# Performance work log

Measured on AMD Instinct MI355X. Metric: run time of the kernel, lower is better.

Reference implementation:

```python
import jax, jax.numpy as jnp
import numpy as np

NEG = -1e9  # stands in for -inf; sparsemax thresholding makes these entries exactly 0


def sparsemax(z):
    """Sparsemax along the last axis (Martins & Astudillo 2016)."""
    K = z.shape[-1]
    z_sorted = -jnp.sort(-z, axis=-1)                      # descending
    kk = jnp.arange(1, K + 1, dtype=z.dtype)
    z_cum = jnp.cumsum(z_sorted, axis=-1)
    support = 1.0 + kk * z_sorted > z_cum                  # [..., K] bool
    k_sup = jnp.sum(support, axis=-1, keepdims=True).astype(z.dtype)
    z_sum = jnp.sum(jnp.where(support, z_sorted, 0.0), axis=-1, keepdims=True)
    tau = (z_sum - 1.0) / k_sup
    return jnp.maximum(z - tau, 0.0)


def setup_inputs() -> dict:
    key = jax.random.key(0)
    ks = jax.random.split(key, 7)
    b, t, e, h = 8, 1024, 128, 8
    x = jax.random.normal(ks[0], (b, t, e), dtype=jnp.float32)
    mask = jax.random.randint(ks[1], (b, t, t), 0, 2, dtype=jnp.int32)
    w_q = jax.random.normal(ks[2], (e, h * e), dtype=jnp.float32) * 0.05
    w_k = jax.random.normal(ks[3], (e, h * e), dtype=jnp.float32) * 0.05
    w_v = jax.random.normal(ks[4], (e, h * e), dtype=jnp.float32) * 0.05
    w_s = jax.random.normal(ks[5], (h, e), dtype=jnp.float32) * 0.05
    b_s = jnp.zeros((h,), dtype=jnp.float32)
    return {"x": x, "mask": mask, "w_q": w_q, "w_k": w_k, "w_v": w_v,
            "w_s": w_s, "b_s": b_s}


def reference(x, mask, w_q, w_k, w_v, w_s, b_s):
    b, t, e = x.shape
    h = w_s.shape[0]
    scale = 1.0 / jnp.sqrt(jnp.asarray(e, x.dtype))  # temperature = emb_dim**0.5

    # projections: each head gets FULL emb_dim width (per original module)
    q = (x @ w_q).reshape(b, t, h, e).transpose(2, 0, 1, 3)  # [h,b,t,e]
    k = (x @ w_k).reshape(b, t, h, e).transpose(2, 0, 1, 3)
    v = (x @ w_v).reshape(b, t, h, e).transpose(2, 0, 1, 3)

    attn = jnp.einsum('hbqe,hbke->hbqk', q * scale, k)       # [h,b,t,t]

    m = mask.astype(bool)[None]                              # [1,b,t,t], broadcast over heads
    inf_mask = jnp.all(m, axis=-1, keepdims=True)            # rows fully masked
    attn = jnp.where(m, NEG, attn)
    attn = jnp.where(inf_mask, 0.0, attn)
    attn = sparsemax(attn)
    attn = jnp.where(inf_mask, 0.0, attn)                    # dropout is identity (p=0)

    out = jnp.einsum('hbqk,hbke->hbqe', attn, v)             # [h,b,t,e]
    out = out.transpose(1, 2, 0, 3)                          # [b,t,h,e]

    sel = jax.nn.softmax(jnp.mean(x, axis=1) @ w_s.T + b_s, axis=-1)  # [b,h]
    return jnp.einsum('bh,bthe->bte', sel, out)              # gated head mix
```

## Files before the change

kernel.cpp:

```cpp
#include <hip/hip_runtime.h>
#include <hip/hip_bf16.h>
#include <math.h>

#define SCALE 0.08838834764831845f

using short8  = __attribute__((ext_vector_type(8))) short;
using short4v = __attribute__((ext_vector_type(4))) short;
using us4     = __attribute__((ext_vector_type(4))) unsigned short;
using f32x4   = __attribute__((ext_vector_type(4))) float;
typedef unsigned long long u64;
typedef unsigned short ushort_t;

static __device__ __forceinline__ ushort_t bf16_of(float f) {
    __hip_bfloat16 h = __float2bfloat16(f);
    return *reinterpret_cast<ushort_t*>(&h);
}
static __device__ __forceinline__ float f_of_bf16(unsigned int u) {
    union { unsigned int i; float f; } v; v.i = u << 16; return v.f;
}

__global__ __launch_bounds__(256)
void prep_all(const float* __restrict__ x, ushort_t* __restrict__ xb,
              const float* __restrict__ wq, const float* __restrict__ wk,
              const float* __restrict__ wv, ushort_t* __restrict__ Wt,
              const int* __restrict__ mask, u64* __restrict__ mp) {
    __shared__ float tile[64][129];
    const int bx = blockIdx.x;
    const int tid = threadIdx.x;
    if (bx < 1024) {
        const int i = bx * 256 + tid;
        float4 v = reinterpret_cast<const float4*>(x)[i];
        short4v o;
        o.x = (short)bf16_of(v.x); o.y = (short)bf16_of(v.y);
        o.z = (short)bf16_of(v.z); o.w = (short)bf16_of(v.w);
        reinterpret_cast<short4v*>(xb)[i] = o;
    } else if (bx < 1072) {
        const int wb = bx - 1024;
        const int mat = wb >> 4;
        const int n0 = (wb & 15) * 64;
        const float* W = (mat == 0) ? wq : (mat == 1) ? wk : wv;
        for (int idx = tid; idx < 8192; idx += 256) {
            const int k = idx >> 6, c = idx & 63;
            tile[c][k] = W[(size_t)k * 1024 + n0 + c];
        }
        __syncthreads();
        for (int idx = tid; idx < 8192; idx += 256) {
            const int c = idx >> 7, k = idx & 127;
            Wt[(size_t)(mat * 1024 + n0 + c) * 128 + k] = bf16_of(tile[c][k]);
        }
    } else {
        const int mb = bx - 1072;
        const int row = mb * 4 + (tid >> 6);
        const int l = tid & 63;
        const int* m = mask + (size_t)row * 1024;
        #pragma unroll
        for (int c = 0; c < 16; ++c) {
            u64 bm = __ballot(m[c * 64 + l] != 0);
            if (l == 0) mp[(size_t)row * 16 + c] = bm;
        }
    }
}

__global__ __launch_bounds__(256)
void proj_gemm(const ushort_t* __restrict__ xb, const ushort_t* __restrict__ Wt,
               ushort_t* __restrict__ Q, ushort_t* __restrict__ K,
               ushort_t* __restrict__ V) {
    const int tid = threadIdx.x;
    const int w = tid >> 6, l = tid & 63;
    const int l15 = l & 15, lq = l >> 4;
    const int m0 = blockIdx.x * 64;
    const int nb = blockIdx.y;
    const int mat = nb >> 4;
    const int n0 = (nb & 15) * 64;
    const int b = m0 >> 10;

    short8 af[4][4];
    #pragma unroll
    for (int at = 0; at < 4; ++at) {
        const ushort_t* ar = xb + (size_t)(m0 + at * 16 + l15) * 128 + lq * 8;
        #pragma unroll
        for (int f = 0; f < 4; ++f)
            af[at][f] = *reinterpret_cast<const short8*>(ar + f * 32);
    }
    const int ng = n0 + w * 16 + l15;
    const ushort_t* br = Wt + (size_t)(mat * 1024 + ng) * 128 + lq * 8;
    short8 bf[4];
    #pragma unroll
    for (int f = 0; f < 4; ++f)
        bf[f] = *reinterpret_cast<const short8*>(br + f * 32);
    f32x4 acc[4];
    #pragma unroll
    for (int at = 0; at < 4; ++at) acc[at] = (f32x4){0.f, 0.f, 0.f, 0.f};
    #pragma unroll
    for (int at = 0; at < 4; ++at)
        #pragma unroll
        for (int f = 0; f < 4; ++f)
            acc[at] = __builtin_amdgcn_mfma_f32_16x16x32_bf16(af[at][f], bf[f], acc[at], 0, 0, 0);

    const int h = ng >> 7, e = ng & 127;
    ushort_t* O = (mat == 0) ? Q : (mat == 1) ? K : V;
    const float scl = (mat == 0) ? SCALE : 1.0f;
    const size_t obase = (size_t)(h * 8 + b) * 131072 + e;
    #pragma unroll
    for (int at = 0; at < 4; ++at)
        #pragma unroll
        for (int r = 0; r < 4; ++r) {
            const int t = (m0 & 1023) + at * 16 + lq * 4 + r;
            O[obase + (size_t)t * 128] = bf16_of(acc[at][r] * scl);
        }
}

__global__ __launch_bounds__(1024)
void sel_kernel(const float* __restrict__ x, const float* __restrict__ wsl,
                const float* __restrict__ bsl, float* __restrict__ sel) {
    __shared__ float part[8][128];
    __shared__ float xm[128];
    __shared__ float lg[8];
    const int b = blockIdx.x;
    const int tid = threadIdx.x;
    const int e = tid & 127, tc = tid >> 7;
    float s = 0.f;
    for (int t = 0; t < 128; ++t)
        s += x[((size_t)b * 1024 + tc * 128 + t) * 128 + e];
    part[tc][e] = s;
    __syncthreads();
    if (tid < 128) {
        float tot = 0.f;
        #pragma unroll
        for (int i = 0; i < 8; ++i) tot += part[i][tid];
        xm[tid] = tot * (1.0f / 1024.0f);
    }
    __syncthreads();
    if (tid < 8) {
        float d = 0.f;
        for (int e2 = 0; e2 < 128; ++e2) d += xm[e2] * wsl[tid * 128 + e2];
        lg[tid] = d + bsl[tid];
    }
    __syncthreads();
    if (tid == 0) {
        float mx = lg[0];
        for (int hh = 1; hh < 8; ++hh) mx = fmaxf(mx, lg[hh]);
        float se = 0.f; float ex[8];
        for (int hh = 0; hh < 8; ++hh) { ex[hh] = expf(lg[hh] - mx); se += ex[hh]; }
        for (int hh = 0; hh < 8; ++hh) sel[b * 8 + hh] = ex[hh] / se;
    }
}

__global__ __launch_bounds__(512, 4)
void attn_kernel(const ushort_t* __restrict__ Qb, const ushort_t* __restrict__ Kb,
                 const ushort_t* __restrict__ Vb, const u64* __restrict__ mp,
                 const float* __restrict__ sel, float* __restrict__ out) {
    __shared__ float S[16 * 1024];
    __shared__ int cnt[16];
    unsigned int* list = reinterpret_cast<unsigned int*>(S);

    const int tid = threadIdx.x;
    const int w = tid >> 6, l = tid & 63;
    const int l15 = l & 15, lq = l >> 4;
    const int orig = (int)blockIdx.x;
    const int swz = (orig & 7) * 64 + (orig >> 3);
    const int b = swz >> 6;
    const int qt = swz & 63;
    const int t0 = qt * 16;
    const int rowbase = b * 1024 + t0;

    const int qrow = 2 * w + (l & 1);
    const int lh = l >> 1;
    const int prow = tid >> 5;
    const int eq = tid & 31;

    if (tid < 16) cnt[tid] = 0;

    u64 mw0[4], mw1[4];
    #pragma unroll
    for (int r = 0; r < 4; ++r) {
        const u64* mrow = mp + (size_t)(rowbase + lq * 4 + r) * 16 + w * 2;
        mw0[r] = mrow[0];
        mw1[r] = mrow[1];
    }

    f32x4 oac = {0.f, 0.f, 0.f, 0.f};

    for (int h = 0; h < 8; ++h) {
        const size_t base = (size_t)(h * 8 + b) * 131072;
        __syncthreads();

        short8 qa[4];
        {
            const ushort_t* qrp = Qb + base + (size_t)(t0 + l15) * 128 + lq * 8;
            #pragma unroll
            for (int f = 0; f < 4; ++f)
                qa[f] = *reinterpret_cast<const short8*>(qrp + f * 32);
        }

        f32x4 sc[8];
        #pragma unroll
        for (int i = 0; i < 8; ++i) {
            const int kt = w * 8 + i;
            const ushort_t* krow = Kb + base + (size_t)(kt * 16 + l15) * 128 + lq * 8;
            f32x4 acc = {0.f, 0.f, 0.f, 0.f};
            #pragma unroll
            for (int f = 0; f < 4; ++f) {
                short8 kb = *reinterpret_cast<const short8*>(krow + f * 32);
                acc = __builtin_amdgcn_mfma_f32_16x16x32_bf16(qa[f], kb, acc, 0, 0, 0);
            }
            sc[i] = acc;
        }

        #pragma unroll
        for (int r = 0; r < 4; ++r) {
            #pragma unroll
            for (int i = 0; i < 8; ++i) {
                const u64 mword = (i < 4) ? mw0[r] : mw1[r];
                const int bit = (i & 3) * 16 + l15;
                if ((mword >> bit) & 1ULL) sc[i][r] = -1e30f;
            }
        }

        #pragma unroll
        for (int r = 0; r < 4; ++r) {
            const int q = lq * 4 + r;
            #pragma unroll
            for (int i = 0; i < 8; ++i) {
                const int c = (w * 8 + i) * 4 + (l15 >> 2);
                const int cp = c ^ ((c >> 3) & 7) ^ (q & 7);
                S[q * 1024 + cp * 4 + (l15 & 3)] = sc[i][r];
            }
        }
        __syncthreads();

        float z[32];
        #pragma unroll
        for (int j = 0; j < 8; ++j) {
            const int c = lh + 32 * j;
            const int cp = c ^ ((c >> 3) & 7) ^ (qrow & 7);
            float4 v = *reinterpret_cast<const float4*>(&S[qrow * 1024 + cp * 4]);
            z[4 * j + 0] = v.x; z[4 * j + 1] = v.y;
            z[4 * j + 2] = v.z; z[4 * j + 3] = v.w;
        }

        float m16[16];
        #pragma unroll
        for (int j = 0; j < 16; ++j) m16[j] = fmaxf(z[j], z[j + 16]);
        #pragma unroll
        for (int j = 0; j < 8; ++j) m16[j] = fmaxf(m16[j], m16[j + 8]);
        #pragma unroll
        for (int j = 0; j < 4; ++j) m16[j] = fmaxf(m16[j], m16[j + 4]);
        float mx = fmaxf(fmaxf(m16[0], m16[1]), fmaxf(m16[2], m16[3]));
        #pragma unroll
        for (int mm = 2; mm < 64; mm <<= 1) mx = fmaxf(mx, __shfl_xor(mx, mm));

        float tau;
        if (mx < -1e29f) {
            tau = 3e38f;
        } else {
            tau = mx - 1.0f;
            unsigned prev = 0xFFFFFFFFu;
            for (int it = 0; it < 64; ++it) {
                float s2 = 0.f; unsigned c2 = 0u;
                #pragma unroll
                for (int k = 0; k < 32; ++k) {
                    const float zz = z[k];
                    s2 += (zz > tau) ? zz : 0.f;
                    c2 += (zz > tau) ? 1u : 0u;
                }
                #pragma unroll
                for (int mm = 2; mm < 64; mm <<= 1) {
                    s2 += __shfl_xor(s2, mm);
                    c2 += __shfl_xor(c2, mm);
                }
                if (c2 == prev) break;
                tau = (s2 - 1.f) / (float)c2;
                prev = c2;
            }
        }

        #pragma unroll
        for (int jj = 0; jj < 32; ++jj) {
            const float p = z[jj] - tau;
            if (p > 0.f) {
                const int k = 4 * lh + 128 * (jj >> 2) + (jj & 3);
                const int pos = atomicAdd(&cnt[qrow], 1);
                list[qrow * 1024 + pos] = (unsigned int)k | ((unsigned int)bf16_of(p) << 16);
            }
        }

        const float gsel = sel[b * 8 + h];
        const int n = cnt[prow];
        const ushort_t* Vrow = Vb + base;
        const unsigned int* lrow = list + prow * 1024;
        for (int j = 0; j < n; ++j) {
            const unsigned int ent = lrow[j];
            const int k = (int)(ent & 0xFFFFu);
            const float gp = gsel * f_of_bf16(ent >> 16);
            us4 vv = *reinterpret_cast<const us4*>(Vrow + (size_t)k * 128 + eq * 4);
            oac[0] += gp * f_of_bf16(vv.x);
            oac[1] += gp * f_of_bf16(vv.y);
            oac[2] += gp * f_of_bf16(vv.z);
            oac[3] += gp * f_of_bf16(vv.w);
        }
        if (eq == 0) cnt[prow] = 0;
    }

    float* orow = out + ((size_t)(b * 1024 + t0 + prow)) * 128 + eq * 4;
    *reinterpret_cast<float4*>(orow) = (float4){oac[0], oac[1], oac[2], oac[3]};
}

extern "C" void kernel_launch(void* const* d_in, const int* in_sizes, int n_in,
                              void* d_out, int out_size, void* d_ws, size_t ws_size,
                              hipStream_t stream) {
    (void)in_sizes; (void)n_in; (void)ws_size; (void)out_size;
    const float* x   = (const float*)d_in[0];
    const int* mask  = (const int*)d_in[1];
    const float* wq  = (const float*)d_in[2];
    const float* wk  = (const float*)d_in[3];
    const float* wv  = (const float*)d_in[4];
    const float* wsl = (const float*)d_in[5];
    const float* bsl = (const float*)d_in[6];
    float* out = (float*)d_out;

    char* wsc = (char*)d_ws;
    float*    sel = (float*)wsc;
    u64*      mp  = (u64*)(wsc + 4096);
    ushort_t* xb  = (ushort_t*)(wsc + 4096 + 1048576);
    ushort_t* Wt  = (ushort_t*)(wsc + 4096 + 1048576 + 2097152);
    ushort_t* Qb  = (ushort_t*)(wsc + 4096 + 1048576 + 2097152 + 786432);
    ushort_t* Kb  = Qb + (size_t)8388608;
    ushort_t* Vb  = Kb + (size_t)8388608;

    prep_all<<<3120, 256, 0, stream>>>(x, xb, wq, wk, wv, Wt, mask, mp);
    sel_kernel<<<8, 1024, 0, stream>>>(x, wsl, bsl, sel);
    proj_gemm<<<dim3(128, 48), 256, 0, stream>>>(xb, Wt, Qb, Kb, Vb);
    attn_kernel<<<512, 512, 0, stream>>>(Qb, Kb, Vb, mp, sel, out);
}
```

Before: 268.1 us.

## Double attention block threads to 1024 with one wave per query row

The attention kernel now launches 1024 threads per block (16 waves). Each wave computes 4 key tiles of scores instead of 8, and owns exactly one query row for the sparsemax threshold search and the sparse V accumulation, so each lane handles 16 scores and 2 output columns. The block-index swizzle is dropped, so consecutive blocks now map to different batches. The change adds thread-level parallelism and shortens each thread's serial work. In exchange it costs more full-wave shuffle reductions and higher register pressure under the tighter launch bounds.

Measured after the change: 328.3 us. +22.4%, slower.

```diff
diff --git a/kernel.cpp b/kernel.cpp
--- a/kernel.cpp
+++ b/kernel.cpp
@@ -6,7 +6,7 @@
 
 using short8  = __attribute__((ext_vector_type(8))) short;
 using short4v = __attribute__((ext_vector_type(4))) short;
-using us4     = __attribute__((ext_vector_type(4))) unsigned short;
+using us2     = __attribute__((ext_vector_type(2))) unsigned short;
 using f32x4   = __attribute__((ext_vector_type(4))) float;
 typedef unsigned long long u64;
 typedef unsigned short ushort_t;
@@ -146,7 +146,7 @@
     }
 }
 
-__global__ __launch_bounds__(512, 4)
+__global__ __launch_bounds__(1024, 8)
 void attn_kernel(const ushort_t* __restrict__ Qb, const ushort_t* __restrict__ Kb,
                  const ushort_t* __restrict__ Vb, const u64* __restrict__ mp,
                  const float* __restrict__ sel, float* __restrict__ out) {
@@ -155,31 +155,23 @@
     unsigned int* list = reinterpret_cast<unsigned int*>(S);
 
     const int tid = threadIdx.x;
-    const int w = tid >> 6, l = tid & 63;
-    const int l15 = l & 15, lq = l >> 4;
+    const int w = tid >> 6;
+    const int l = tid & 63;
+    const int l15 = l & 15, lq = (l >> 4) & 3;
     const int orig = (int)blockIdx.x;
-    const int swz = (orig & 7) * 64 + (orig >> 3);
-    const int b = swz >> 6;
-    const int qt = swz & 63;
+    const int b = orig & 7;
+    const int qt = orig >> 3;
     const int t0 = qt * 16;
     const int rowbase = b * 1024 + t0;
 
-    const int qrow = 2 * w + (l & 1);
-    const int lh = l >> 1;
-    const int prow = tid >> 5;
-    const int eq = tid & 31;
-
     if (tid < 16) cnt[tid] = 0;
 
-    u64 mw0[4], mw1[4];
-    #pragma unroll
-    for (int r = 0; r < 4; ++r) {
-        const u64* mrow = mp + (size_t)(rowbase + lq * 4 + r) * 16 + w * 2;
-        mw0[r] = mrow[0];
-        mw1[r] = mrow[1];
-    }
-
-    f32x4 oac = {0.f, 0.f, 0.f, 0.f};
+    u64 mw[4];
+    #pragma unroll
+    for (int r = 0; r < 4; ++r)
+        mw[r] = mp[(size_t)(rowbase + lq * 4 + r) * 16 + w];
+
+    float o0 = 0.f, o1 = 0.f;
 
     for (int h = 0; h < 8; ++h) {
         const size_t base = (size_t)(h * 8 + b) * 131072;
@@ -193,10 +185,10 @@
                 qa[f] = *reinterpret_cast<const short8*>(qrp + f * 32);
         }
 
-        f32x4 sc[8];
-        #pragma unroll
-        for (int i = 0; i < 8; ++i) {
-            const int kt = w * 8 + i;
+        f32x4 sc[4];
+        #pragma unroll
+        for (int i = 0; i < 4; ++i) {
+            const int kt = 4 * w + i;
             const ushort_t* krow = Kb + base + (size_t)(kt * 16 + l15) * 128 + lq * 8;
             f32x4 acc = {0.f, 0.f, 0.f, 0.f};
             #pragma unroll
@@ -210,10 +202,9 @@
         #pragma unroll
         for (int r = 0; r < 4; ++r) {
             #pragma unroll
-            for (int i = 0; i < 8; ++i) {
-                const u64 mword = (i < 4) ? mw0[r] : mw1[r];
-                const int bit = (i & 3) * 16 + l15;
-                if ((mword >> bit) & 1ULL) sc[i][r] = -1e30f;
+            for (int i = 0; i < 4; ++i) {
+                const int bit = i * 16 + l15;
+                if ((mw[r] >> bit) & 1ULL) sc[i][r] = -1e30f;
             }
         }
 
@@ -221,34 +212,32 @@
         for (int r = 0; r < 4; ++r) {
             const int q = lq * 4 + r;
             #pragma unroll
-            for (int i = 0; i < 8; ++i) {
-                const int c = (w * 8 + i) * 4 + (l15 >> 2);
+            for (int i = 0; i < 4; ++i) {
+                const int c = 16 * w + 4 * i + (l15 >> 2);
                 const int cp = c ^ ((c >> 3) & 7) ^ (q & 7);
                 S[q * 1024 + cp * 4 + (l15 & 3)] = sc[i][r];
             }
         }
         __syncthreads();
 
-        float z[32];
-        #pragma unroll
-        for (int j = 0; j < 8; ++j) {
-            const int c = lh + 32 * j;
-            const int cp = c ^ ((c >> 3) & 7) ^ (qrow & 7);
-            float4 v = *reinterpret_cast<const float4*>(&S[qrow * 1024 + cp * 4]);
+        float z[16];
+        #pragma unroll
+        for (int j = 0; j < 4; ++j) {
+            const int c = l + 64 * j;
+            const int cp = c ^ ((c >> 3) & 7) ^ (w & 7);
+            float4 v = *reinterpret_cast<const float4*>(&S[w * 1024 + cp * 4]);
             z[4 * j + 0] = v.x; z[4 * j + 1] = v.y;
             z[4 * j + 2] = v.z; z[4 * j + 3] = v.w;
         }
 
-        float m16[16];
-        #pragma unroll
-        for (int j = 0; j < 16; ++j) m16[j] = fmaxf(z[j], z[j + 16]);
-        #pragma unroll
-        for (int j = 0; j < 8; ++j) m16[j] = fmaxf(m16[j], m16[j + 8]);
-        #pragma unroll
-        for (int j = 0; j < 4; ++j) m16[j] = fmaxf(m16[j], m16[j + 4]);
-        float mx = fmaxf(fmaxf(m16[0], m16[1]), fmaxf(m16[2], m16[3]));
-        #pragma unroll
-        for (int mm = 2; mm < 64; mm <<= 1) mx = fmaxf(mx, __shfl_xor(mx, mm));
+        float m8[8];
+        #pragma unroll
+        for (int j = 0; j < 8; ++j) m8[j] = fmaxf(z[j], z[j + 8]);
+        #pragma unroll
+        for (int j = 0; j < 4; ++j) m8[j] = fmaxf(m8[j], m8[j + 4]);
+        float mx = fmaxf(fmaxf(m8[0], m8[1]), fmaxf(m8[2], m8[3]));
+        #pragma unroll
+        for (int mm = 1; mm < 64; mm <<= 1) mx = fmaxf(mx, __shfl_xor(mx, mm));
 
         float tau;
         if (mx < -1e29f) {
@@ -259,13 +248,13 @@
             for (int it = 0; it < 64; ++it) {
                 float s2 = 0.f; unsigned c2 = 0u;
                 #pragma unroll
-                for (int k = 0; k < 32; ++k) {
+                for (int k = 0; k < 16; ++k) {
                     const float zz = z[k];
                     s2 += (zz > tau) ? zz : 0.f;
                     c2 += (zz > tau) ? 1u : 0u;
                 }
                 #pragma unroll
-                for (int mm = 2; mm < 64; mm <<= 1) {
+                for (int mm = 1; mm < 64; mm <<= 1) {
                     s2 += __shfl_xor(s2, mm);
                     c2 += __shfl_xor(c2, mm);
                 }
@@ -276,34 +265,32 @@
         }
 
         #pragma unroll
-        for (int jj = 0; jj < 32; ++jj) {
+        for (int jj = 0; jj < 16; ++jj) {
             const float p = z[jj] - tau;
             if (p > 0.f) {
-                const int k = 4 * lh + 128 * (jj >> 2) + (jj & 3);
-                const int pos = atomicAdd(&cnt[qrow], 1);
-                list[qrow * 1024 + pos] = (unsigned int)k | ((unsigned int)bf16_of(p) << 16);
+                const int k = 4 * l + 256 * (jj >> 2) + (jj & 3);
+                const int pos = atomicAdd(&cnt[w], 1);
+                list[w * 1024 + pos] = (unsigned int)k | ((unsigned int)bf16_of(p) << 16);
             }
         }
 
         const float gsel = sel[b * 8 + h];
-        const int n = cnt[prow];
+        const int n = cnt[w];
         const ushort_t* Vrow = Vb + base;
-        const unsigned int* lrow = list + prow * 1024;
+        const unsigned int* lrow = list + w * 1024;
         for (int j = 0; j < n; ++j) {
             const unsigned int ent = lrow[j];
             const int k = (int)(ent & 0xFFFFu);
             const float gp = gsel * f_of_bf16(ent >> 16);
-            us4 vv = *reinterpret_cast<const us4*>(Vrow + (size_t)k * 128 + eq * 4);
-            oac[0] += gp * f_of_bf16(vv.x);
-            oac[1] += gp * f_of_bf16(vv.y);
-            oac[2] += gp * f_of_bf16(vv.z);
-            oac[3] += gp * f_of_bf16(vv.w);
-        }
-        if (eq == 0) cnt[prow] = 0;
-    }
-
-    float* orow = out + ((size_t)(b * 1024 + t0 + prow)) * 128 + eq * 4;
-    *reinterpret_cast<float4*>(orow) = (float4){oac[0], oac[1], oac[2], oac[3]};
+            us2 vv = *reinterpret_cast<const us2*>(Vrow + (size_t)k * 128 + 2 * l);
+            o0 += gp * f_of_bf16(vv.x);
+            o1 += gp * f_of_bf16(vv.y);
+        }
+        if (l == 0) cnt[w] = 0;
+    }
+
+    float* orow = out + ((size_t)(b * 1024 + t0 + w)) * 128 + 2 * l;
+    *reinterpret_cast<float2*>(orow) = (float2){o0, o1};
 }
 
 extern "C" void kernel_launch(void* const* d_in, const int* in_sizes, int n_in,
@@ -331,5 +318,5 @@
     prep_all<<<3120, 256, 0, stream>>>(x, xb, wq, wk, wv, Wt, mask, mp);
     sel_kernel<<<8, 1024, 0, stream>>>(x, wsl, bsl, sel);
     proj_gemm<<<dim3(128, 48), 256, 0, stream>>>(xb, Wt, Qb, Kb, Vb);
-    attn_kernel<<<512, 512, 0, stream>>>(Qb, Kb, Vb, mp, sel, out);
-}
+    attn_kernel<<<512, 1024, 0, stream>>>(Qb, Kb, Vb, mp, sel, out);
+}
```

## Prefetch next head's QK scores, fuse x-mean into prep, unroll PV gather

Applied to the files above, without the earlier changes.

The attention kernel now computes the QK^T MFMA scores for the next head while the current head's sparsemax and PV gather run, giving the two phases a chance to overlap. The x column-mean reduction for the head selector is moved into the prep kernel via shared and global atomics, replacing the standalone strided sel_kernel with a small finalize kernel plus a memset. The sparse PV gather loop is unrolled by two with separate accumulators to raise memory-level parallelism. In exchange, register pressure rises from the extra scn buffer, which may hurt occupancy, and the float atomic summation order becomes nondeterministic.

New measurement: 373.2 us. +39.2%, slower.

```diff
diff --git a/kernel.cpp b/kernel.cpp
--- a/kernel.cpp
+++ b/kernel.cpp
@@ -23,8 +23,10 @@
 void prep_all(const float* __restrict__ x, ushort_t* __restrict__ xb,
               const float* __restrict__ wq, const float* __restrict__ wk,
               const float* __restrict__ wv, ushort_t* __restrict__ Wt,
-              const int* __restrict__ mask, u64* __restrict__ mp) {
+              const int* __restrict__ mask, u64* __restrict__ mp,
+              float* __restrict__ xsum) {
     __shared__ float tile[64][129];
+    __shared__ float csum[128];
     const int bx = blockIdx.x;
     const int tid = threadIdx.x;
     if (bx < 1024) {
@@ -34,6 +36,15 @@
         o.x = (short)bf16_of(v.x); o.y = (short)bf16_of(v.y);
         o.z = (short)bf16_of(v.z); o.w = (short)bf16_of(v.w);
         reinterpret_cast<short4v*>(xb)[i] = o;
+        if (tid < 128) csum[tid] = 0.f;
+        __syncthreads();
+        const int e0 = (tid & 31) * 4;
+        atomicAdd(&csum[e0 + 0], v.x);
+        atomicAdd(&csum[e0 + 1], v.y);
+        atomicAdd(&csum[e0 + 2], v.z);
+        atomicAdd(&csum[e0 + 3], v.w);
+        __syncthreads();
+        if (tid < 128) atomicAdd(&xsum[(bx >> 7) * 128 + tid], csum[tid]);
     } else if (bx < 1072) {
         const int wb = bx - 1024;
         const int mat = wb >> 4;
@@ -110,30 +121,18 @@
         }
 }
 
-__global__ __launch_bounds__(1024)
-void sel_kernel(const float* __restrict__ x, const float* __restrict__ wsl,
-                const float* __restrict__ bsl, float* __restrict__ sel) {
-    __shared__ float part[8][128];
+__global__ __launch_bounds__(128)
+void sel_final(const float* __restrict__ xsum, const float* __restrict__ wsl,
+               const float* __restrict__ bsl, float* __restrict__ sel) {
     __shared__ float xm[128];
     __shared__ float lg[8];
     const int b = blockIdx.x;
     const int tid = threadIdx.x;
-    const int e = tid & 127, tc = tid >> 7;
-    float s = 0.f;
-    for (int t = 0; t < 128; ++t)
-        s += x[((size_t)b * 1024 + tc * 128 + t) * 128 + e];
-    part[tc][e] = s;
-    __syncthreads();
-    if (tid < 128) {
-        float tot = 0.f;
-        #pragma unroll
-        for (int i = 0; i < 8; ++i) tot += part[i][tid];
-        xm[tid] = tot * (1.0f / 1024.0f);
-    }
+    xm[tid] = xsum[b * 128 + tid] * (1.0f / 1024.0f);
     __syncthreads();
     if (tid < 8) {
         float d = 0.f;
-        for (int e2 = 0; e2 < 128; ++e2) d += xm[e2] * wsl[tid * 128 + e2];
+        for (int e = 0; e < 128; ++e) d += xm[e] * wsl[tid * 128 + e];
         lg[tid] = d + bsl[tid];
     }
     __syncthreads();
@@ -179,25 +178,18 @@
         mw1[r] = mrow[1];
     }
 
-    f32x4 oac = {0.f, 0.f, 0.f, 0.f};
-
-    for (int h = 0; h < 8; ++h) {
-        const size_t base = (size_t)(h * 8 + b) * 131072;
-        __syncthreads();
-
+    f32x4 sc[8];
+    {
+        const size_t base0 = (size_t)b * 131072;
         short8 qa[4];
-        {
-            const ushort_t* qrp = Qb + base + (size_t)(t0 + l15) * 128 + lq * 8;
-            #pragma unroll
-            for (int f = 0; f < 4; ++f)
-                qa[f] = *reinterpret_cast<const short8*>(qrp + f * 32);
-        }
-
-        f32x4 sc[8];
+        const ushort_t* qrp = Qb + base0 + (size_t)(t0 + l15) * 128 + lq * 8;
+        #pragma unroll
+        for (int f = 0; f < 4; ++f)
+            qa[f] = *reinterpret_cast<const short8*>(qrp + f * 32);
         #pragma unroll
         for (int i = 0; i < 8; ++i) {
             const int kt = w * 8 + i;
-            const ushort_t* krow = Kb + base + (size_t)(kt * 16 + l15) * 128 + lq * 8;
+            const ushort_t* krow = Kb + base0 + (size_t)(kt * 16 + l15) * 128 + lq * 8;
             f32x4 acc = {0.f, 0.f, 0.f, 0.f};
             #pragma unroll
             for (int f = 0; f < 4; ++f) {
@@ -206,6 +198,13 @@
             }
             sc[i] = acc;
         }
+    }
+
+    f32x4 oac = {0.f, 0.f, 0.f, 0.f};
+
+    #pragma unroll
+    for (int h = 0; h < 8; ++h) {
+        const size_t base = (size_t)(h * 8 + b) * 131072;
 
         #pragma unroll
         for (int r = 0; r < 4; ++r) {
@@ -216,6 +215,8 @@
                 if ((mword >> bit) & 1ULL) sc[i][r] = -1e30f;
             }
         }
+
+        __syncthreads();
 
         #pragma unroll
         for (int r = 0; r < 4; ++r) {
@@ -237,6 +238,28 @@
             float4 v = *reinterpret_cast<const float4*>(&S[qrow * 1024 + cp * 4]);
             z[4 * j + 0] = v.x; z[4 * j + 1] = v.y;
             z[4 * j + 2] = v.z; z[4 * j + 3] = v.w;
+        }
+
+        f32x4 scn[8];
+        if (h < 7) {
+            const size_t nbase = (size_t)((h + 1) * 8 + b) * 131072;
+            short8 qn[4];
+            const ushort_t* qrp = Qb + nbase + (size_t)(t0 + l15) * 128 + lq * 8;
+            #pragma unroll
+            for (int f = 0; f < 4; ++f)
+                qn[f] = *reinterpret_cast<const short8*>(qrp + f * 32);
+            #pragma unroll
+            for (int i = 0; i < 8; ++i) {
+                const int kt = w * 8 + i;
+                const ushort_t* krow = Kb + nbase + (size_t)(kt * 16 + l15) * 128 + lq * 8;
+                f32x4 acc = {0.f, 0.f, 0.f, 0.f};
+                #pragma unroll
+                for (int f = 0; f < 4; ++f) {
+                    short8 kb = *reinterpret_cast<const short8*>(krow + f * 32);
+                    acc = __builtin_amdgcn_mfma_f32_16x16x32_bf16(qn[f], kb, acc, 0, 0, 0);
+                }
+                scn[i] = acc;
+            }
         }
 
         float m16[16];
@@ -289,17 +312,40 @@
         const int n = cnt[prow];
         const ushort_t* Vrow = Vb + base;
         const unsigned int* lrow = list + prow * 1024;
-        for (int j = 0; j < n; ++j) {
-            const unsigned int ent = lrow[j];
-            const int k = (int)(ent & 0xFFFFu);
-            const float gp = gsel * f_of_bf16(ent >> 16);
-            us4 vv = *reinterpret_cast<const us4*>(Vrow + (size_t)k * 128 + eq * 4);
-            oac[0] += gp * f_of_bf16(vv.x);
-            oac[1] += gp * f_of_bf16(vv.y);
-            oac[2] += gp * f_of_bf16(vv.z);
-            oac[3] += gp * f_of_bf16(vv.w);
-        }
+        float a0 = 0.f, a1 = 0.f, a2 = 0.f, a3 = 0.f;
+        float b0 = 0.f, b1 = 0.f, b2 = 0.f, b3 = 0.f;
+        int j = 0;
+        for (; j + 2 <= n; j += 2) {
+            const unsigned int e0 = lrow[j];
+            const unsigned int e1 = lrow[j + 1];
+            const int k0 = (int)(e0 & 0xFFFFu);
+            const int k1 = (int)(e1 & 0xFFFFu);
+            const float g0 = gsel * f_of_bf16(e0 >> 16);
+            const float g1 = gsel * f_of_bf16(e1 >> 16);
+            us4 v0 = *reinterpret_cast<const us4*>(Vrow + (size_t)k0 * 128 + eq * 4);
+            us4 v1 = *reinterpret_cast<const us4*>(Vrow + (size_t)k1 * 128 + eq * 4);
+            a0 += g0 * f_of_bf16(v0.x); a1 += g0 * f_of_bf16(v0.y);
+            a2 += g0 * f_of_bf16(v0.z); a3 += g0 * f_of_bf16(v0.w);
+            b0 += g1 * f_of_bf16(v1.x); b1 += g1 * f_of_bf16(v1.y);
+            b2 += g1 * f_of_bf16(v1.z); b3 += g1 * f_of_bf16(v1.w);
+        }
+        if (j < n) {
+            const unsigned int e0 = lrow[j];
+            const int k0 = (int)(e0 & 0xFFFFu);
+            const float g0 = gsel * f_of_bf16(e0 >> 16);
+            us4 v0 = *reinterpret_cast<const us4*>(Vrow + (size_t)k0 * 128 + eq * 4);
+            a0 += g0 * f_of_bf16(v0.x); a1 += g0 * f_of_bf16(v0.y);
+            a2 += g0 * f_of_bf16(v0.z); a3 += g0 * f_of_bf16(v0.w);
+        }
+        oac[0] += a0 + b0; oac[1] += a1 + b1;
+        oac[2] += a2 + b2; oac[3] += a3 + b3;
+
         if (eq == 0) cnt[prow] = 0;
+
+        if (h < 7) {
+            #pragma unroll
+            for (int i = 0; i < 8; ++i) sc[i] = scn[i];
+        }
     }
 
     float* orow = out + ((size_t)(b * 1024 + t0 + prow)) * 128 + eq * 4;
@@ -320,16 +366,18 @@
     float* out = (float*)d_out;
 
     char* wsc = (char*)d_ws;
-    float*    sel = (float*)wsc;
-    u64*      mp  = (u64*)(wsc + 4096);
-    ushort_t* xb  = (ushort_t*)(wsc + 4096 + 1048576);
-    ushort_t* Wt  = (ushort_t*)(wsc + 4096 + 1048576 + 2097152);
-    ushort_t* Qb  = (ushort_t*)(wsc + 4096 + 1048576 + 2097152 + 786432);
-    ushort_t* Kb  = Qb + (size_t)8388608;
-    ushort_t* Vb  = Kb + (size_t)8388608;
-
-    prep_all<<<3120, 256, 0, stream>>>(x, xb, wq, wk, wv, Wt, mask, mp);
-    sel_kernel<<<8, 1024, 0, stream>>>(x, wsl, bsl, sel);
+    float*    sel  = (float*)wsc;
+    float*    xsum = (float*)(wsc + 1024);
+    u64*      mp   = (u64*)(wsc + 8192);
+    ushort_t* xb   = (ushort_t*)(wsc + 8192 + 1048576);
+    ushort_t* Wt   = (ushort_t*)(wsc + 8192 + 1048576 + 2097152);
+    ushort_t* Qb   = (ushort_t*)(wsc + 8192 + 1048576 + 2097152 + 786432);
+    ushort_t* Kb   = Qb + (size_t)8388608;
+    ushort_t* Vb   = Kb + (size_t)8388608;
+
+    hipMemsetAsync(xsum, 0, 4096, stream);
+    prep_all<<<3120, 256, 0, stream>>>(x, xb, wq, wk, wv, Wt, mask, mp, xsum);
     proj_gemm<<<dim3(128, 48), 256, 0, stream>>>(xb, Wt, Qb, Kb, Vb);
+    sel_final<<<8, 128, 0, stream>>>(xsum, wsl, bsl, sel);
     attn_kernel<<<512, 512, 0, stream>>>(Qb, Kb, Vb, mp, sel, out);
 }
```
